# Performance work log

Hardware: AMD Instinct MI355X
Metric: run time of the kernel (lower is better)

The kernel has to match this reference:

```python
import jax, jax.numpy as jnp
import numpy as np

N = 50000      # nodes
DEG = 32       # fixed out-degree used to build a synthetic CSR graph
E = N * DEG    # edges
F = 64         # in_feats = n_hidden = out_feats
K = 3          # n_kernels
DIM = 2        # pseudo-coordinate projection dim
L = 3          # n_layers + 1 GMMConv layers


def setup_inputs() -> dict:
    key = jax.random.key(0)
    ks = jax.random.split(key, 8)
    feat = jax.random.normal(ks[0], (N, F), jnp.float32)
    pseudo = jax.random.uniform(ks[1], (E, 2), jnp.float32)  # per-edge pseudo coords
    rowptr = jnp.arange(N + 1, dtype=jnp.int32) * DEG        # CSR row pointers
    colind = jax.random.randint(ks[2], (E,), 0, N, jnp.int32)  # neighbor (src) ids
    # Per-layer parameters, stacked over L layers (all layers are FxF here).
    proj_W = 0.5 * jax.random.normal(ks[3], (L, 2, DIM), jnp.float32)   # pseudo_proj Linear weight
    proj_b = jnp.zeros((L, DIM), jnp.float32)                            # pseudo_proj Linear bias
    fc_W = jax.random.normal(ks[4], (L, F, K * F), jnp.float32) / np.sqrt(F)  # GMMConv fc (no bias)
    mu = jax.random.normal(ks[5], (L, K, DIM), jnp.float32)              # Gaussian means
    inv_sigma = jnp.ones((L, K, DIM), jnp.float32)                       # inverse std-devs
    return {"feat": feat, "pseudo": pseudo, "rowptr": rowptr, "colind": colind,
            "proj_W": proj_W, "proj_b": proj_b, "fc_W": fc_W, "mu": mu,
            "inv_sigma": inv_sigma}


def reference(feat, pseudo, rowptr, colind, proj_W, proj_b, fc_W, mu, inv_sigma):
    n = feat.shape[0]
    e = colind.shape[0]
    n_layers = fc_W.shape[0]
    n_kern = mu.shape[1]
    # dst node of each edge from CSR rowptr (edge e belongs to row i iff rowptr[i] <= e < rowptr[i+1])
    dst = jnp.searchsorted(rowptr, jnp.arange(e, dtype=rowptr.dtype), side="right") - 1

    h = feat
    for i in range(n_layers):  # small fixed layer loop
        # pseudo_proj: Linear(2, dim) + Tanh, per edge -> [E, DIM]
        u = jnp.tanh(pseudo @ proj_W[i] + proj_b[i])
        # Gaussian kernel weights: w[e,k] = exp(-0.5 * sum_d ((u - mu)^2 * inv_sigma^2)) -> [E, K]
        diff = u[:, None, :] - mu[i][None, :, :]
        w = jnp.exp(-0.5 * jnp.sum(diff * diff * (inv_sigma[i][None, :, :] ** 2), axis=-1))
        out_dim = fc_W[i].shape[1] // n_kern
        hp = (h @ fc_W[i]).reshape(n, n_kern, out_dim)  # [N, K, out]
        # message per edge: sum_k w[e,k] * hp[src(e), k, :]; loop over small K to avoid [E,K,out]
        msg = jnp.zeros((e, out_dim), h.dtype)
        for k in range(n_kern):
            msg = msg + w[:, k:k + 1] * hp[colind, k, :]
        # scatter-reduce (sum aggregation) into destination nodes
        h = jax.ops.segment_sum(msg, dst, num_segments=n)
        # dropout is identity in eval mode (p=0.0)
    return h
```

## Files before the change

kernel.cpp:

```cpp
#include <hip/hip_runtime.h>
#include <math.h>

#define FEAT 64
#define NKERN 3

typedef __attribute__((ext_vector_type(8))) short short8;
typedef __attribute__((ext_vector_type(4))) float float4v;
typedef __attribute__((ext_vector_type(2))) float float2v;

__device__ __forceinline__ unsigned short f2bf(float f) {
    unsigned int u = __float_as_uint(f);
    u = (u + 0x7fffu + ((u >> 16) & 1u)) >> 16;
    return (unsigned short)u;
}
__device__ __forceinline__ float bf2f(unsigned short b) {
    return __uint_as_float(((unsigned int)b) << 16);
}
__device__ __forceinline__ float fast_tanh(float x) {
    float e = __expf(2.f * x);
    return fmaf(-2.f, __builtin_amdgcn_rcpf(e + 1.f), 1.f);
}

__global__ __launch_bounds__(256) void prep_kernel(
    const float* __restrict__ x, unsigned short* __restrict__ y, int n4,
    const float* __restrict__ fcW,
    unsigned short* __restrict__ Bth, unsigned short* __restrict__ Btl,
    int totalW, int nCastBlocks)
{
    int b = blockIdx.x;
    if (b < nCastBlocks) {
        int i = b * 256 + threadIdx.x;
        if (i >= n4) return;
        float4 v = ((const float4*)x)[i];
        ushort4 o;
        o.x = f2bf(v.x); o.y = f2bf(v.y); o.z = f2bf(v.z); o.w = f2bf(v.w);
        ((ushort4*)y)[i] = o;
    } else {
        int idx = (b - nCastBlocks) * 256 + threadIdx.x;
        if (idx >= totalW) return;
        int l   = idx / (FEAT * 192);
        int rem = idx - l * (FEAT * 192);
        int f   = rem / 192;
        int jp  = rem - f * 192;
        int k = jp >> 6, j = jp & 63;
        float v = fcW[(size_t)l * 12288 + j * 192 + k * 64 + f];
        unsigned short hi = f2bf(v);
        int dst = l * 12288 +
                  ((((f >> 4) * 6 + (jp >> 5)) * 4 + ((jp >> 3) & 3)) * 16 + (f & 15)) * 8 +
                  (jp & 7);
        Bth[dst] = hi;
        Btl[dst] = f2bf(v - bf2f(hi));
    }
}

__global__ __launch_bounds__(256, 4) void layer_kernel(
    const unsigned short* __restrict__ h,
    const int*   __restrict__ rowptr,
    const int*   __restrict__ colind,
    const float* __restrict__ pseudo,
    const float* __restrict__ projW,
    const float* __restrict__ projB,
    const float* __restrict__ mu,
    const float* __restrict__ isg,
    int layer,
    const unsigned short* __restrict__ Bth,
    const unsigned short* __restrict__ Btl,
    float* __restrict__ out,
    unsigned short* __restrict__ hnext,
    int n_nodes, int last_layer)
{
    __shared__ __align__(16) unsigned short Atile[3264];
    __shared__ __align__(16) unsigned int   WldsU[4][2][132];
    int tid  = threadIdx.x;
    int wv   = tid >> 6;
    int lane = tid & 63;
    int t0   = blockIdx.x * 16;

    const float* pw = projW + layer * 4;
    const float* pb = projB + layer * 2;
    const float* mm = mu  + layer * 6;
    const float* ss = isg + layer * 6;
    float pw0 = pw[0], pw1 = pw[1], pw2 = pw[2], pw3 = pw[3];
    float pb0 = pb[0], pb1 = pb[1];
    float m0 = mm[0], m1 = mm[1], m2 = mm[2], m3 = mm[3], m4 = mm[4], m5 = mm[5];
    float c0 = -0.5f * ss[0] * ss[0], c1 = -0.5f * ss[1] * ss[1];
    float c2 = -0.5f * ss[2] * ss[2], c3 = -0.5f * ss[3] * ss[3];
    float c4 = -0.5f * ss[4] * ss[4], c5 = -0.5f * ss[5] * ss[5];

    int half = lane >> 5;
    int p    = lane & 31;
    unsigned int featoff = (unsigned int)(p * 4);
    const char* hb = (const char*)h;

    for (int s2 = 0; s2 < 2; ++s2) {
        int nA    = t0 + wv * 4 + s2 * 2;
        int nodeh = nA + half;
        int ncl   = nodeh < n_nodes - 1 ? nodeh : (n_nodes - 1);
        int rp    = rowptr[ncl];
        int deg   = rowptr[ncl + 1] - rp;
        bool fast = __all((deg == 32) && (nodeh < n_nodes));

        if (fast) {
            int ei = rp + p;
            int cc = colind[ei];
            float2 ps = ((const float2*)pseudo)[ei];
            float u0 = fast_tanh(fmaf(ps.x, pw0, fmaf(ps.y, pw2, pb0)));
            float u1 = fast_tanh(fmaf(ps.x, pw1, fmaf(ps.y, pw3, pb1)));
            float d0 = u0 - m0, d1 = u1 - m1;
            float w0v = __expf(fmaf(d0 * d0, c0, d1 * d1 * c1));
            d0 = u0 - m2; d1 = u1 - m3;
            float w1v = __expf(fmaf(d0 * d0, c2, d1 * d1 * c3));
            d0 = u0 - m4; d1 = u1 - m5;
            float w2v = __expf(fmaf(d0 * d0, c4, d1 * d1 * c5));
            uint4 recw;
            recw.x = ((unsigned int)cc) << 7;
            recw.y = __float_as_uint(w0v);
            recw.z = __float_as_uint(w1v);
            recw.w = __float_as_uint(w2v);
            *(uint4*)&WldsU[wv][half][p * 4] = recw;

            float2v a0 = {0.f, 0.f}, a1 = {0.f, 0.f}, a2 = {0.f, 0.f};
            const unsigned int* Wrec = &WldsU[wv][half][0];
            #pragma unroll
            for (int i = 0; i < 32; ++i) {
                uint4 rec = *(const uint4*)(Wrec + i * 4);
                unsigned int hv = *(const unsigned int*)(hb + (rec.x + featoff));
                float2v vf;
                vf.x = __uint_as_float(hv << 16);
                vf.y = __uint_as_float(hv & 0xffff0000u);
                float w0 = __uint_as_float(rec.y);
                float w1 = __uint_as_float(rec.z);
                float w2 = __uint_as_float(rec.w);
#if __has_builtin(__builtin_elementwise_fma)
                float2v w0s = {w0, w0}, w1s = {w1, w1}, w2s = {w2, w2};
                a0 = __builtin_elementwise_fma(vf, w0s, a0);
                a1 = __builtin_elementwise_fma(vf, w1s, a1);
                a2 = __builtin_elementwise_fma(vf, w2s, a2);
#else
                a0.x = fmaf(vf.x, w0, a0.x); a0.y = fmaf(vf.y, w0, a0.y);
                a1.x = fmaf(vf.x, w1, a1.x); a1.y = fmaf(vf.y, w1, a1.y);
                a2.x = fmaf(vf.x, w2, a2.x); a2.y = fmaf(vf.y, w2, a2.y);
#endif
            }
            int m  = wv * 4 + s2 * 2 + half;
            int j0 = p * 2;
            int sa = (j0 >> 5) * 544 + ((j0 >> 3) & 3) * 136 + m * 8 + (j0 & 7);
            unsigned int pk0, pk1, pk2;
            asm("v_cvt_pk_bf16_f32 %0, %1, %2" : "=v"(pk0) : "v"(a0.x), "v"(a0.y));
            asm("v_cvt_pk_bf16_f32 %0, %1, %2" : "=v"(pk1) : "v"(a1.x), "v"(a1.y));
            asm("v_cvt_pk_bf16_f32 %0, %1, %2" : "=v"(pk2) : "v"(a2.x), "v"(a2.y));
            *(unsigned int*)&Atile[sa]        = pk0;
            *(unsigned int*)&Atile[sa + 1088] = pk1;
            *(unsigned int*)&Atile[sa + 2176] = pk2;
        } else {
            for (int t = 0; t < 2; ++t) {
                int node = nA + t;
                float a0 = 0.f, a1 = 0.f, a2 = 0.f;
                if (node < n_nodes) {
                    int nu = __builtin_amdgcn_readfirstlane(node);
                    int r0 = rowptr[nu];
                    int dg = rowptr[nu + 1] - r0;
                    for (int i = 0; i < dg; ++i) {
                        int cc = colind[r0 + i];
                        float px = pseudo[(size_t)(r0 + i) * 2];
                        float py = pseudo[(size_t)(r0 + i) * 2 + 1];
                        float u0 = fast_tanh(fmaf(px, pw0, fmaf(py, pw2, pb0)));
                        float u1 = fast_tanh(fmaf(px, pw1, fmaf(py, pw3, pb1)));
                        float d0 = u0 - m0, d1 = u1 - m1;
                        float w0e = __expf(fmaf(d0 * d0, c0, d1 * d1 * c1));
                        d0 = u0 - m2; d1 = u1 - m3;
                        float w1e = __expf(fmaf(d0 * d0, c2, d1 * d1 * c3));
                        d0 = u0 - m4; d1 = u1 - m5;
                        float w2e = __expf(fmaf(d0 * d0, c4, d1 * d1 * c5));
                        float vf = bf2f(h[(size_t)cc * FEAT + lane]);
                        a0 = fmaf(w0e, vf, a0);
                        a1 = fmaf(w1e, vf, a1);
                        a2 = fmaf(w2e, vf, a2);
                    }
                }
                int m  = wv * 4 + s2 * 2 + t;
                int sb = (lane >> 5) * 544 + ((lane >> 3) & 3) * 136 + m * 8 + (lane & 7);
                Atile[sb]        = f2bf(a0);
                Atile[sb + 1088] = f2bf(a1);
                Atile[sb + 2176] = f2bf(a2);
            }
        }
    }
    __syncthreads();

    int q  = lane >> 4;
    int nn = lane & 15;
    const unsigned short* bt0 = Bth + (((wv * 6) * 4 + q) * 16 + nn) * 8;
    const unsigned short* bt1 = Btl + (((wv * 6) * 4 + q) * 16 + nn) * 8;
    float4v acc = (float4v){0.f, 0.f, 0.f, 0.f};
    #pragma unroll
    for (int ks = 0; ks < 6; ++ks) {
        short8 ah = *(const short8*)&Atile[ks * 544 + q * 136 + nn * 8];
        short8 bh = *(const short8*)(bt0 + ks * 512);
        short8 bl = *(const short8*)(bt1 + ks * 512);
        acc = __builtin_amdgcn_mfma_f32_16x16x32_bf16(ah, bh, acc, 0, 0, 0);
        acc = __builtin_amdgcn_mfma_f32_16x16x32_bf16(ah, bl, acc, 0, 0, 0);
    }
    #pragma unroll
    for (int r = 0; r < 4; ++r) {
        int row = t0 + q * 4 + r;
        if (row < n_nodes) {
            if (last_layer)
                out[(size_t)row * 64 + wv * 16 + nn] = acc[r];
            else
                hnext[(size_t)row * 64 + wv * 16 + nn] = f2bf(acc[r]);
        }
    }
}

extern "C" void kernel_launch(void* const* d_in, const int* in_sizes, int n_in,
                              void* d_out, int out_size, void* d_ws, size_t ws_size,
                              hipStream_t stream)
{
    const float* feat   = (const float*)d_in[0];
    const float* pseudo = (const float*)d_in[1];
    const int*   rowptr = (const int*)d_in[2];
    const int*   colind = (const int*)d_in[3];
    const float* projW  = (const float*)d_in[4];
    const float* projB  = (const float*)d_in[5];
    const float* fcW    = (const float*)d_in[6];
    const float* mu     = (const float*)d_in[7];
    const float* isg    = (const float*)d_in[8];
    float* out = (float*)d_out;

    int n  = in_sizes[0] / FEAT;
    int n_layers = in_sizes[6] / (FEAT * NKERN * FEAT);

    unsigned short* hbA = (unsigned short*)d_ws;
    unsigned short* hbB = hbA + (size_t)n * FEAT;
    unsigned short* Bth = hbB + (size_t)n * FEAT;
    unsigned short* Btl = Bth + (size_t)n_layers * 12288;

    int n4 = n * FEAT / 4;
    int totalW = n_layers * FEAT * 192;
    int castBlocks = (n4 + 255) / 256;
    int wpBlocks   = (totalW + 255) / 256;

    dim3 blk(256);
    dim3 prepGrid(castBlocks + wpBlocks);
    dim3 layerGrid((n + 15) / 16);
    dim3 layerBlk(256);

    prep_kernel<<<prepGrid, blk, 0, stream>>>(
        feat, hbA, n4, fcW, Bth, Btl, totalW, castBlocks);

    const unsigned short* hin = hbA;
    for (int l = 0; l < n_layers; ++l) {
        int last = (l == n_layers - 1);
        unsigned short* hb_out = (l == 0) ? hbB : hbA;
        layer_kernel<<<layerGrid, layerBlk, 0, stream>>>(
            hin, rowptr, colind, pseudo, projW, projB, mu, isg, l,
            Bth + (size_t)l * 12288, Btl + (size_t)l * 12288,
            out, hb_out, n, last);
        hin = hb_out;
    }
}
```

Before: 167.8 us.

## Gather four nodes per wave with 8-byte feature loads and 4-edge batches

Edge weights for all four of a wave's nodes are computed up front into a larger LDS buffer. The aggregation then lets 16 lanes cover one node, with each lane loading 8 bytes (4 bf16 features) per neighbor. Edges are processed four at a time, and the next group's LDS records are prefetched so several gathers are in flight at once. The goal is fewer, wider memory instructions and more memory-level parallelism, at the cost of more registers and a slow path that now covers all four nodes whenever either pair is irregular.

```diff
diff --git a/kernel.cpp b/kernel.cpp
--- a/kernel.cpp
+++ b/kernel.cpp
@@ -70,7 +70,7 @@
     int n_nodes, int last_layer)
 {
     __shared__ __align__(16) unsigned short Atile[3264];
-    __shared__ __align__(16) unsigned int   WldsU[4][2][132];
+    __shared__ __align__(16) unsigned int   Wlds[4][4][132];
     int tid  = threadIdx.x;
     int wv   = tid >> 6;
     int lane = tid & 63;
@@ -89,17 +89,17 @@
 
     int half = lane >> 5;
     int p    = lane & 31;
-    unsigned int featoff = (unsigned int)(p * 4);
     const char* hb = (const char*)h;
 
-    for (int s2 = 0; s2 < 2; ++s2) {
-        int nA    = t0 + wv * 4 + s2 * 2;
-        int nodeh = nA + half;
-        int ncl   = nodeh < n_nodes - 1 ? nodeh : (n_nodes - 1);
-        int rp    = rowptr[ncl];
-        int deg   = rowptr[ncl + 1] - rp;
-        bool fast = __all((deg == 32) && (nodeh < n_nodes));
-
+    bool fastp[2];
+    #pragma unroll
+    for (int tt = 0; tt < 2; ++tt) {
+        int node = t0 + wv * 4 + tt * 2 + half;
+        int ncl  = node < n_nodes - 1 ? node : (n_nodes - 1);
+        int rp   = rowptr[ncl];
+        int deg  = rowptr[ncl + 1] - rp;
+        bool fast = __all((deg == 32) && (node < n_nodes));
+        fastp[tt] = fast;
         if (fast) {
             int ei = rp + p;
             int cc = colind[ei];
@@ -117,73 +117,107 @@
             recw.y = __float_as_uint(w0v);
             recw.z = __float_as_uint(w1v);
             recw.w = __float_as_uint(w2v);
-            *(uint4*)&WldsU[wv][half][p * 4] = recw;
-
-            float2v a0 = {0.f, 0.f}, a1 = {0.f, 0.f}, a2 = {0.f, 0.f};
-            const unsigned int* Wrec = &WldsU[wv][half][0];
-            #pragma unroll
-            for (int i = 0; i < 32; ++i) {
-                uint4 rec = *(const uint4*)(Wrec + i * 4);
-                unsigned int hv = *(const unsigned int*)(hb + (rec.x + featoff));
-                float2v vf;
-                vf.x = __uint_as_float(hv << 16);
-                vf.y = __uint_as_float(hv & 0xffff0000u);
-                float w0 = __uint_as_float(rec.y);
-                float w1 = __uint_as_float(rec.z);
-                float w2 = __uint_as_float(rec.w);
-#if __has_builtin(__builtin_elementwise_fma)
-                float2v w0s = {w0, w0}, w1s = {w1, w1}, w2s = {w2, w2};
-                a0 = __builtin_elementwise_fma(vf, w0s, a0);
-                a1 = __builtin_elementwise_fma(vf, w1s, a1);
-                a2 = __builtin_elementwise_fma(vf, w2s, a2);
-#else
-                a0.x = fmaf(vf.x, w0, a0.x); a0.y = fmaf(vf.y, w0, a0.y);
-                a1.x = fmaf(vf.x, w1, a1.x); a1.y = fmaf(vf.y, w1, a1.y);
-                a2.x = fmaf(vf.x, w2, a2.x); a2.y = fmaf(vf.y, w2, a2.y);
-#endif
+            *(uint4*)&Wlds[wv][tt * 2 + half][p * 4] = recw;
+        }
+    }
+
+    if (fastp[0] && fastp[1]) {
+        int g  = lane >> 4;
+        int p4 = lane & 15;
+        unsigned int fo4 = (unsigned int)(p4 * 8);
+        const unsigned int* Wg = &Wlds[wv][g][0];
+
+        float2v a0l = {0.f,0.f}, a0h = {0.f,0.f};
+        float2v a1l = {0.f,0.f}, a1h = {0.f,0.f};
+        float2v a2l = {0.f,0.f}, a2h = {0.f,0.f};
+
+        uint4 r0 = *(const uint4*)(Wg + 0);
+        uint4 r1 = *(const uint4*)(Wg + 4);
+        uint4 r2 = *(const uint4*)(Wg + 8);
+        uint4 r3 = *(const uint4*)(Wg + 12);
+
+        #pragma unroll
+        for (int b = 0; b < 8; ++b) {
+            uint2 h0 = *(const uint2*)(hb + (r0.x + fo4));
+            uint2 h1 = *(const uint2*)(hb + (r1.x + fo4));
+            uint2 h2 = *(const uint2*)(hb + (r2.x + fo4));
+            uint2 h3 = *(const uint2*)(hb + (r3.x + fo4));
+            uint4 n0, n1, n2, n3;
+            if (b < 7) {
+                n0 = *(const uint4*)(Wg + (b + 1) * 16 + 0);
+                n1 = *(const uint4*)(Wg + (b + 1) * 16 + 4);
+                n2 = *(const uint4*)(Wg + (b + 1) * 16 + 8);
+                n3 = *(const uint4*)(Wg + (b + 1) * 16 + 12);
             }
-            int m  = wv * 4 + s2 * 2 + half;
-            int j0 = p * 2;
-            int sa = (j0 >> 5) * 544 + ((j0 >> 3) & 3) * 136 + m * 8 + (j0 & 7);
-            unsigned int pk0, pk1, pk2;
-            asm("v_cvt_pk_bf16_f32 %0, %1, %2" : "=v"(pk0) : "v"(a0.x), "v"(a0.y));
-            asm("v_cvt_pk_bf16_f32 %0, %1, %2" : "=v"(pk1) : "v"(a1.x), "v"(a1.y));
-            asm("v_cvt_pk_bf16_f32 %0, %1, %2" : "=v"(pk2) : "v"(a2.x), "v"(a2.y));
-            *(unsigned int*)&Atile[sa]        = pk0;
-            *(unsigned int*)&Atile[sa + 1088] = pk1;
-            *(unsigned int*)&Atile[sa + 2176] = pk2;
-        } else {
-            for (int t = 0; t < 2; ++t) {
-                int node = nA + t;
-                float a0 = 0.f, a1 = 0.f, a2 = 0.f;
-                if (node < n_nodes) {
-                    int nu = __builtin_amdgcn_readfirstlane(node);
-                    int r0 = rowptr[nu];
-                    int dg = rowptr[nu + 1] - r0;
-                    for (int i = 0; i < dg; ++i) {
-                        int cc = colind[r0 + i];
-                        float px = pseudo[(size_t)(r0 + i) * 2];
-                        float py = pseudo[(size_t)(r0 + i) * 2 + 1];
-                        float u0 = fast_tanh(fmaf(px, pw0, fmaf(py, pw2, pb0)));
-                        float u1 = fast_tanh(fmaf(px, pw1, fmaf(py, pw3, pb1)));
-                        float d0 = u0 - m0, d1 = u1 - m1;
-                        float w0e = __expf(fmaf(d0 * d0, c0, d1 * d1 * c1));
-                        d0 = u0 - m2; d1 = u1 - m3;
-                        float w1e = __expf(fmaf(d0 * d0, c2, d1 * d1 * c3));
-                        d0 = u0 - m4; d1 = u1 - m5;
-                        float w2e = __expf(fmaf(d0 * d0, c4, d1 * d1 * c5));
-                        float vf = bf2f(h[(size_t)cc * FEAT + lane]);
-                        a0 = fmaf(w0e, vf, a0);
-                        a1 = fmaf(w1e, vf, a1);
-                        a2 = fmaf(w2e, vf, a2);
-                    }
+#define CONSUME(hv, rc) do {                                                   \
+            float2v vlo, vhi;                                                  \
+            vlo.x = __uint_as_float((hv).x << 16);                             \
+            vlo.y = __uint_as_float((hv).x & 0xffff0000u);                     \
+            vhi.x = __uint_as_float((hv).y << 16);                             \
+            vhi.y = __uint_as_float((hv).y & 0xffff0000u);                     \
+            float w0 = __uint_as_float((rc).y);                                \
+            float w1 = __uint_as_float((rc).z);                                \
+            float w2 = __uint_as_float((rc).w);                                \
+            float2v s0 = {w0, w0}, s1 = {w1, w1}, s2 = {w2, w2};               \
+            a0l = __builtin_elementwise_fma(vlo, s0, a0l);                     \
+            a0h = __builtin_elementwise_fma(vhi, s0, a0h);                     \
+            a1l = __builtin_elementwise_fma(vlo, s1, a1l);                     \
+            a1h = __builtin_elementwise_fma(vhi, s1, a1h);                     \
+            a2l = __builtin_elementwise_fma(vlo, s2, a2l);                     \
+            a2h = __builtin_elementwise_fma(vhi, s2, a2h);                     \
+        } while (0)
+            CONSUME(h0, r0);
+            CONSUME(h1, r1);
+            CONSUME(h2, r2);
+            CONSUME(h3, r3);
+#undef CONSUME
+            if (b < 7) { r0 = n0; r1 = n1; r2 = n2; r3 = n3; }
+        }
+
+        int m  = wv * 4 + g;
+        int j0 = p4 * 4;
+        int sa = (j0 >> 5) * 544 + ((j0 >> 3) & 3) * 136 + m * 8 + (j0 & 7);
+        unsigned int k0l, k0h, k1l, k1h, k2l, k2h;
+        asm("v_cvt_pk_bf16_f32 %0, %1, %2" : "=v"(k0l) : "v"(a0l.x), "v"(a0l.y));
+        asm("v_cvt_pk_bf16_f32 %0, %1, %2" : "=v"(k0h) : "v"(a0h.x), "v"(a0h.y));
+        asm("v_cvt_pk_bf16_f32 %0, %1, %2" : "=v"(k1l) : "v"(a1l.x), "v"(a1l.y));
+        asm("v_cvt_pk_bf16_f32 %0, %1, %2" : "=v"(k1h) : "v"(a1h.x), "v"(a1h.y));
+        asm("v_cvt_pk_bf16_f32 %0, %1, %2" : "=v"(k2l) : "v"(a2l.x), "v"(a2l.y));
+        asm("v_cvt_pk_bf16_f32 %0, %1, %2" : "=v"(k2h) : "v"(a2h.x), "v"(a2h.y));
+        uint2 w0 = {k0l, k0h}, w1 = {k1l, k1h}, w2 = {k2l, k2h};
+        *(uint2*)&Atile[sa]        = w0;
+        *(uint2*)&Atile[sa + 1088] = w1;
+        *(uint2*)&Atile[sa + 2176] = w2;
+    } else {
+        for (int mq = 0; mq < 4; ++mq) {
+            int node = t0 + wv * 4 + mq;
+            float a0 = 0.f, a1 = 0.f, a2 = 0.f;
+            if (node < n_nodes) {
+                int nu = __builtin_amdgcn_readfirstlane(node);
+                int r0 = rowptr[nu];
+                int dg = rowptr[nu + 1] - r0;
+                for (int i = 0; i < dg; ++i) {
+                    int cc = colind[r0 + i];
+                    float px = pseudo[(size_t)(r0 + i) * 2];
+                    float py = pseudo[(size_t)(r0 + i) * 2 + 1];
+                    float u0 = fast_tanh(fmaf(px, pw0, fmaf(py, pw2, pb0)));
+                    float u1 = fast_tanh(fmaf(px, pw1, fmaf(py, pw3, pb1)));
+                    float d0 = u0 - m0, d1 = u1 - m1;
+                    float w0e = __expf(fmaf(d0 * d0, c0, d1 * d1 * c1));
+                    d0 = u0 - m2; d1 = u1 - m3;
+                    float w1e = __expf(fmaf(d0 * d0, c2, d1 * d1 * c3));
+                    d0 = u0 - m4; d1 = u1 - m5;
+                    float w2e = __expf(fmaf(d0 * d0, c4, d1 * d1 * c5));
+                    float vf = bf2f(h[(size_t)cc * FEAT + lane]);
+                    a0 = fmaf(w0e, vf, a0);
+                    a1 = fmaf(w1e, vf, a1);
+                    a2 = fmaf(w2e, vf, a2);
                 }
-                int m  = wv * 4 + s2 * 2 + t;
-                int sb = (lane >> 5) * 544 + ((lane >> 3) & 3) * 136 + m * 8 + (lane & 7);
-                Atile[sb]        = f2bf(a0);
-                Atile[sb + 1088] = f2bf(a1);
-                Atile[sb + 2176] = f2bf(a2);
             }
+            int sb = (lane >> 5) * 544 + ((lane >> 3) & 3) * 136 + (wv * 4 + mq) * 8 + (lane & 7);
+            Atile[sb]        = f2bf(a0);
+            Atile[sb + 1088] = f2bf(a1);
+            Atile[sb + 2176] = f2bf(a2);
         }
     }
     __syncthreads();
```

Result: no change. 167.0 us (-0.5%).
